# Kernel optimization log

Measured on AMD Instinct MI355X. Metric: run time of the kernel, lower is better.

## Reference

```python
import jax, jax.numpy as jnp
import numpy as np

EPS = 1e-5

def _ln(x, g=None, b=None):
    m = jnp.mean(x, axis=-1, keepdims=True)
    v = jnp.var(x, axis=-1, keepdims=True)
    y = (x - m) / jnp.sqrt(v + EPS)
    if g is not None:
        y = y * g + b
    return y

def setup_inputs() -> dict:
    key = jax.random.key(0)
    B, N, C = 2, 2048, 1024   # batch, tokens, query_dim
    H, D = 16, 64             # heads, dim_head -> inner = 1024
    inner = H * D
    ks = jax.random.split(key, 8)
    s = C ** -0.5
    inp = {
        'x':   jax.random.normal(ks[0], (B, N, C), jnp.float32),
        'w_q': jax.random.normal(ks[1], (C, inner), jnp.float32) * s,
        'b_q': jnp.zeros((inner,), jnp.float32),
        'w_k': jax.random.normal(ks[2], (C, inner), jnp.float32) * s,
        'b_k': jnp.zeros((inner,), jnp.float32),
        'w_v': jax.random.normal(ks[3], (C, inner), jnp.float32) * s,
        'b_v': jnp.zeros((inner,), jnp.float32),
        'g_q': jnp.ones((inner,), jnp.float32),
        'be_q': jnp.zeros((inner,), jnp.float32),
        'g_k': jnp.ones((inner,), jnp.float32),
        'be_k': jnp.zeros((inner,), jnp.float32),
        # to_out is zero-initialized in the torch code; use small random weights
        # so forward/backward are non-trivial for correctness testing.
        'w_o': jax.random.normal(ks[4], (inner, C), jnp.float32) * s,
        'b_o': jnp.zeros((C,), jnp.float32),
    }
    return inp

def reference(x, w_q, b_q, w_k, b_k, w_v, b_v, g_q, be_q, g_k, be_k, w_o, b_o):
    B, N, C = x.shape
    inner = w_q.shape[1]
    H = 16
    D = inner // H
    xn = _ln(x)                                  # pre-norm, no affine
    ctx = xn                                     # self-attention (context=None)
    silu = jax.nn.silu
    q = silu(xn) @ w_q + b_q                     # [B,N,inner]
    k = silu(ctx) @ w_k + b_k
    v = silu(ctx) @ w_v + b_v
    q = _ln(q, g_q, be_q)
    k = _ln(k, g_k, be_k)
    q = q * (inner ** -0.5)                      # NB: scale by inner_dim, pre-split
    q = q.reshape(B, N, H, D)
    k = k.reshape(B, N, H, D)
    v = v.reshape(B, N, H, D)
    w = jnp.einsum('bihd,bjhd->bhij', q, k)      # [B,H,N,N]
    w = jax.nn.softmax(w, axis=-1)
    o = jnp.einsum('bhij,bjhd->bihd', w, v).reshape(B, N, inner)
    return silu(o) @ w_o + b_o
```

## Files before the change

kernel.cpp:

```cpp
#include <hip/hip_runtime.h>
#include <hip/hip_bf16.h>
#include <math.h>

#define LN_EPS 1e-5f

typedef __attribute__((ext_vector_type(8))) short bf16x8;
typedef __attribute__((ext_vector_type(8))) short short8;
typedef __attribute__((ext_vector_type(4))) float f32x4;
typedef unsigned short ushort_t;

__device__ __forceinline__ float silu_f(float x) {
    return x / (1.0f + __expf(-x));
}

__device__ __forceinline__ ushort_t f2bf(float f) {
    __hip_bfloat16 h = __float2bfloat16(f);
    return *reinterpret_cast<ushort_t*>(&h);
}

__device__ __forceinline__ float bf2f(ushort_t u) {
    __hip_bfloat16 h = *reinterpret_cast<__hip_bfloat16*>(&u);
    return __bfloat162float(h);
}

__device__ __forceinline__ unsigned pk2(float a, float b) {
    unsigned r;
    asm("v_cvt_pk_bf16_f32 %0, %1, %2" : "=v"(r) : "v"(a), "v"(b));
    return r;
}

__device__ __forceinline__ float fast_exp2(float x) {
#if defined(__has_builtin)
#if __has_builtin(__builtin_amdgcn_exp2f)
    return __builtin_amdgcn_exp2f(x);
#else
    return exp2f(x);
#endif
#else
    return exp2f(x);
#endif
}

__device__ __forceinline__ void gld16(const void* g, void* lds) {
    __builtin_amdgcn_global_load_lds(
        (const __attribute__((address_space(1))) unsigned int*)g,
        (__attribute__((address_space(3))) unsigned int*)lds, 16, 0, 0);
}

__device__ __forceinline__ float2 block_reduce2(float2 p, float2* sbuf) {
    #pragma unroll
    for (int off = 32; off > 0; off >>= 1) {
        p.x += __shfl_down(p.x, off, 64);
        p.y += __shfl_down(p.y, off, 64);
    }
    int lane = threadIdx.x & 63;
    int wid  = threadIdx.x >> 6;
    if (lane == 0) sbuf[wid] = p;
    __syncthreads();
    if (threadIdx.x == 0) {
        float2 r = sbuf[0];
        for (int i = 1; i < 4; ++i) { r.x += sbuf[i].x; r.y += sbuf[i].y; }
        sbuf[0] = r;
    }
    __syncthreads();
    return sbuf[0];
}

__global__ __launch_bounds__(256) void ln_silu_kernel(
    const float* __restrict__ x, ushort_t* __restrict__ out)
{
    __shared__ float2 sbuf[4];
    const int C = 1024;
    int row = blockIdx.x;
    const float4* xr = (const float4*)(x + (size_t)row * C);
    float4 v = xr[threadIdx.x];
    float2 p;
    p.x = v.x + v.y + v.z + v.w;
    p.y = v.x*v.x + v.y*v.y + v.z*v.z + v.w*v.w;
    float2 s = block_reduce2(p, sbuf);
    float mean = s.x / (float)C;
    float var  = s.y / (float)C - mean * mean;
    float rstd = rsqrtf(var + LN_EPS);
    ushort4 y;
    y.x = f2bf(silu_f((v.x - mean) * rstd));
    y.y = f2bf(silu_f((v.y - mean) * rstd));
    y.z = f2bf(silu_f((v.z - mean) * rstd));
    y.w = f2bf(silu_f((v.w - mean) * rstd));
    ((ushort4*)(out + (size_t)row * C))[threadIdx.x] = y;
}

__global__ __launch_bounds__(256) void ln_affine_bf16(
    ushort_t* __restrict__ qk0, ushort_t* __restrict__ qk1,
    const float* __restrict__ g0, const float* __restrict__ be0,
    const float* __restrict__ g1, const float* __restrict__ be1,
    float scale0, float scale1)
{
    __shared__ float2 sbuf[4];
    const int C = 1024;
    int which = blockIdx.y;
    ushort_t* q = which ? qk1 : qk0;
    const float* g  = which ? g1  : g0;
    const float* be = which ? be1 : be0;
    float scale = which ? scale1 : scale0;
    int row = blockIdx.x;
    ushort4 u = ((ushort4*)(q + (size_t)row * C))[threadIdx.x];
    float v0 = bf2f(u.x), v1 = bf2f(u.y), v2 = bf2f(u.z), v3 = bf2f(u.w);
    float2 p;
    p.x = v0 + v1 + v2 + v3;
    p.y = v0*v0 + v1*v1 + v2*v2 + v3*v3;
    float2 s = block_reduce2(p, sbuf);
    float mean = s.x / (float)C;
    float var  = s.y / (float)C - mean * mean;
    float rstd = rsqrtf(var + LN_EPS);
    float4 gv = ((const float4*)g)[threadIdx.x];
    float4 bv = ((const float4*)be)[threadIdx.x];
    ushort4 y;
    y.x = f2bf(((v0 - mean) * rstd * gv.x + bv.x) * scale);
    y.y = f2bf(((v1 - mean) * rstd * gv.y + bv.y) * scale);
    y.z = f2bf(((v2 - mean) * rstd * gv.z + bv.z) * scale);
    y.w = f2bf(((v3 - mean) * rstd * gv.w + bv.w) * scale);
    ((ushort4*)(q + (size_t)row * C))[threadIdx.x] = y;
}

struct W4 { const float* p[4]; };

__global__ __launch_bounds__(256) void transpose_w(W4 w, ushort_t* __restrict__ outbase)
{
    __shared__ float Ls[64][65];
    int z = blockIdx.z;
    const float* in = w.p[z];
    ushort_t* out = outbase + (size_t)z * 1024 * 1024;
    int r0 = blockIdx.y * 64, c0 = blockIdx.x * 64;
    int t = threadIdx.x, r = t >> 2, j = (t & 3) * 16;
    #pragma unroll
    for (int i = 0; i < 4; ++i) {
        float4 v = *(const float4*)(in + (size_t)(r0 + r) * 1024 + c0 + j + i * 4);
        Ls[r][j + i*4 + 0] = v.x;
        Ls[r][j + i*4 + 1] = v.y;
        Ls[r][j + i*4 + 2] = v.z;
        Ls[r][j + i*4 + 3] = v.w;
    }
    __syncthreads();
    __align__(16) ushort_t tmp[16];
    #pragma unroll
    for (int i = 0; i < 16; ++i) tmp[i] = f2bf(Ls[j + i][r]);
    ushort_t* op = out + (size_t)(c0 + r) * 1024 + r0 + j;
    *(short8*)(op)     = *(short8*)(tmp);
    *(short8*)(op + 8) = *(short8*)(tmp + 8);
}

template<int BM, bool OUT_BF16>
__global__ __launch_bounds__(256) void gemm_mfma(
    const ushort_t* __restrict__ A, const ushort_t* __restrict__ Bt0,
    const float* __restrict__ b0, const float* __restrict__ b1,
    const float* __restrict__ b2, void* __restrict__ out0,
    ushort_t* __restrict__ vt_out,
    int M, int N, int K)
{
    constexpr int BK = 64;
    constexpr int MI = BM / 32;
    __shared__ ushort_t Smem[(BM + 128) * BK];
    ushort_t* As = Smem;
    ushort_t* Bs = Smem + BM * BK;

    int z = blockIdx.z;
    const ushort_t* Bt = Bt0 + (size_t)z * N * K;
    const float* bias = (z == 0) ? b0 : (z == 1) ? b1 : b2;

    int t = threadIdx.x;
    int lane = t & 63, wv = t >> 6;
    int wr = wv >> 1, wc = wv & 1;
    int quad = lane >> 4, ln16 = lane & 15;

    int row0 = blockIdx.y * BM;
    int col0 = blockIdx.x * 128;

    const f32x4 zero4 = {0.f, 0.f, 0.f, 0.f};
    f32x4 acc[MI][4];
    #pragma unroll
    for (int i = 0; i < MI; ++i)
        #pragma unroll
        for (int j = 0; j < 4; ++j) acc[i][j] = zero4;

    for (int kt = 0; kt < K; kt += BK) {
        #pragma unroll
        for (int c = 0; c < BM / 32; ++c) {
            int idx = c * 256 + t;
            int r = idx >> 3, ch = idx & 7;
            int g = ch ^ (r & 7);
            gld16(A + (size_t)(row0 + r) * K + kt + g * 8,
                  As + (size_t)(c * 256 + wv * 64) * 8);
        }
        #pragma unroll
        for (int c = 0; c < 4; ++c) {
            int idx = c * 256 + t;
            int r = idx >> 3, ch = idx & 7;
            int g = ch ^ (r & 7);
            gld16(Bt + (size_t)(col0 + r) * K + kt + g * 8,
                  Bs + (size_t)(c * 256 + wv * 64) * 8);
        }
        __syncthreads();
        #pragma unroll
        for (int s = 0; s < 2; ++s) {
            bf16x8 af[MI], bf[4];
            int g = s * 4 + quad;
            #pragma unroll
            for (int i = 0; i < MI; ++i) {
                int m = wr * (BM / 2) + i * 16 + ln16;
                af[i] = *(const bf16x8*)(As + (size_t)(m * 8 + (g ^ (m & 7))) * 8);
            }
            #pragma unroll
            for (int j = 0; j < 4; ++j) {
                int n = wc * 64 + j * 16 + ln16;
                bf[j] = *(const bf16x8*)(Bs + (size_t)(n * 8 + (g ^ (n & 7))) * 8);
            }
            #pragma unroll
            for (int i = 0; i < MI; ++i)
                #pragma unroll
                for (int j = 0; j < 4; ++j)
                    acc[i][j] = __builtin_amdgcn_mfma_f32_16x16x32_bf16(
                        af[i], bf[j], acc[i][j], 0, 0, 0);
        }
        __syncthreads();
    }

    if (OUT_BF16 && z == 2 && BM == 128) {
        ushort_t* tb = Smem + wv * 4096;
        int tok0 = row0 + wr * 64;
        int chn0 = col0 + wc * 64;
        #pragma unroll
        for (int j = 0; j < 4; ++j) {
            int chl = j * 16 + ln16;
            float bv = bias[chn0 + chl];
            #pragma unroll
            for (int i = 0; i < MI; ++i) {
                uint2 uu;
                uu.x = pk2(acc[i][j][0] + bv, acc[i][j][1] + bv);
                uu.y = pk2(acc[i][j][2] + bv, acc[i][j][3] + bv);
                int hc = i * 4 + quad;
                int phys = hc ^ ((chl & 7) << 1);
                *(uint2*)(tb + chl * 64 + phys * 4) = uu;
            }
        }
        int bb2 = tok0 >> 11;
        int tokb = tok0 & 2047;
        #pragma unroll
        for (int p = 0; p < 8; ++p) {
            int chl = p * 8 + (lane >> 3);
            int tc  = lane & 7;
            int ptc = tc ^ (chl & 7);
            uint4 vvv = *(const uint4*)(tb + chl * 64 + ptc * 8);
            *(uint4*)(vt_out + ((size_t)bb2 * 1024 + chn0 + chl) * 2048 + tokb + tc * 8) = vvv;
        }
    } else {
        #pragma unroll
        for (int j = 0; j < 4; ++j) {
            int col = col0 + wc * 64 + j * 16 + ln16;
            float bv = bias[col];
            #pragma unroll
            for (int i = 0; i < MI; ++i) {
                int rowb = row0 + wr * (BM / 2) + i * 16 + quad * 4;
                #pragma unroll
                for (int r = 0; r < 4; ++r) {
                    float val = acc[i][j][r] + bv;
                    if (OUT_BF16) {
                        ushort_t* out = (ushort_t*)out0 + (size_t)z * M * N;
                        out[(size_t)(rowb + r) * N + col] = f2bf(val);
                    } else {
                        float* out = (float*)out0;
                        out[(size_t)(rowb + r) * N + col] = val;
                    }
                }
            }
        }
    }
}

__global__ __launch_bounds__(256, 4) void flash_mfma(
    const ushort_t* __restrict__ qb, const ushort_t* __restrict__ kb,
    const ushort_t* __restrict__ vT, ushort_t* __restrict__ ob)
{
    const int N = 2048, HD = 1024, D = 64, H = 16;
    const int KT = 64;
    const int NT = N / KT;
    __shared__ ushort_t Ks[2][64 * 64];
    __shared__ ushort_t Vs[2][64 * 64];

    int t = threadIdx.x, lane = t & 63, wv = t >> 6;
    int quad = lane >> 4, ln16 = lane & 15;
    int qt = blockIdx.x, h = blockIdx.y, b = blockIdx.z;

    size_t qk_base = (size_t)b * N * HD + (size_t)h * D;
    size_t vt_base = (size_t)(b * H + h) * D * N;

    bf16x8 qf[2];
    {
        const ushort_t* qp = qb + qk_base + (size_t)(qt * 64 + wv * 16 + ln16) * HD;
        qf[0] = *(const bf16x8*)(qp + quad * 8);
        qf[1] = *(const bf16x8*)(qp + 32 + quad * 8);
    }

    bf16x8 ones;
    #pragma unroll
    for (int i = 0; i < 8; ++i) ones[i] = (short)0x3F80;

    const f32x4 zero4 = {0.f, 0.f, 0.f, 0.f};
    f32x4 oacc[4];
    f32x4 lacc = zero4;
    #pragma unroll
    for (int j = 0; j < 4; ++j) oacc[j] = zero4;

    auto stage_K = [&](ushort_t* KsB, int kt) {
        #pragma unroll
        for (int c = 0; c < 2; ++c) {
            int idx = c * 256 + t;
            int r = idx >> 3, ch = idx & 7, g = ch ^ (r & 7);
            int pr = (r & ~31) | (((r >> 2) & 3) << 3) | (((r >> 4) & 1) << 2) | (r & 3);
            gld16(kb + qk_base + (size_t)(kt + pr) * HD + g * 8,
                  KsB + (size_t)(c * 256 + wv * 64) * 8);
        }
    };
    auto stage_V = [&](ushort_t* VsB, int kt) {
        #pragma unroll
        for (int c = 0; c < 2; ++c) {
            int idx = c * 256 + t;
            int r = idx >> 3, ch = idx & 7, g = ch ^ (r & 7);
            gld16(vT + vt_base + (size_t)r * N + kt + g * 8,
                  VsB + (size_t)(c * 256 + wv * 64) * 8);
        }
    };

    auto qk_tile = [&](const ushort_t* KsB, f32x4 (&st)[4]) {
        #pragma unroll
        for (int j = 0; j < 4; ++j) st[j] = zero4;
        __builtin_amdgcn_s_setprio(1);
        #pragma unroll
        for (int s = 0; s < 2; ++s) {
            int g = s * 4 + quad;
            #pragma unroll
            for (int j = 0; j < 4; ++j) {
                int n = j * 16 + ln16;
                bf16x8 kf = *(const bf16x8*)(KsB + ((size_t)n * 8 + (g ^ (n & 7))) * 8);
                st[j] = __builtin_amdgcn_mfma_f32_16x16x32_bf16(kf, qf[s], st[j], 0, 0, 0);
            }
        }
        __builtin_amdgcn_s_setprio(0);
    };

    auto sm_pv = [&](f32x4 (&st)[4], const ushort_t* VsB) {
        bf16x8 vf[2][4];
        #pragma unroll
        for (int w = 0; w < 2; ++w) {
            int phys = (w * 4 + quad) ^ (ln16 & 7);
            #pragma unroll
            for (int mt = 0; mt < 4; ++mt)
                vf[w][mt] = *(const bf16x8*)(VsB + (size_t)(mt * 16 + ln16) * 64 + phys * 8);
        }
        #pragma unroll
        for (int j = 0; j < 4; ++j) {
            st[j][0] = fast_exp2(st[j][0]);
            st[j][1] = fast_exp2(st[j][1]);
            st[j][2] = fast_exp2(st[j][2]);
            st[j][3] = fast_exp2(st[j][3]);
        }
        #pragma unroll
        for (int w = 0; w < 2; ++w) {
            uint4 up;
            up.x = pk2(st[2*w][0],   st[2*w][1]);
            up.y = pk2(st[2*w][2],   st[2*w][3]);
            up.z = pk2(st[2*w+1][0], st[2*w+1][1]);
            up.w = pk2(st[2*w+1][2], st[2*w+1][3]);
            bf16x8 pf = __builtin_bit_cast(bf16x8, up);
            __builtin_amdgcn_s_setprio(1);
            lacc = __builtin_amdgcn_mfma_f32_16x16x32_bf16(ones, pf, lacc, 0, 0, 0);
            #pragma unroll
            for (int mt = 0; mt < 4; ++mt)
                oacc[mt] = __builtin_amdgcn_mfma_f32_16x16x32_bf16(vf[w][mt], pf, oacc[mt], 0, 0, 0);
            __builtin_amdgcn_s_setprio(0);
        }
    };

    f32x4 stA[4], stB[4];

    stage_K(Ks[0], 0);       stage_V(Vs[0], 0);
    stage_K(Ks[1], KT);      stage_V(Vs[1], KT);
    asm volatile("s_waitcnt vmcnt(4)" ::: "memory");
    __builtin_amdgcn_s_barrier();
    __builtin_amdgcn_sched_barrier(0);
    qk_tile(Ks[0], stA);
    __builtin_amdgcn_sched_barrier(0);
    __builtin_amdgcn_s_barrier();

    #pragma unroll 1
    for (int it = 0; it < NT - 2; it += 2) {
        stage_K(Ks[0], (it + 2) * KT);
        asm volatile("s_waitcnt vmcnt(4)" ::: "memory");
        __builtin_amdgcn_s_barrier();
        __builtin_amdgcn_sched_barrier(0);
        qk_tile(Ks[1], stB);
        sm_pv(stA, Vs[0]);
        __builtin_amdgcn_sched_barrier(0);
        __builtin_amdgcn_s_barrier();
        stage_V(Vs[0], (it + 2) * KT);

        stage_K(Ks[1], (it + 3) * KT);
        asm volatile("s_waitcnt vmcnt(4)" ::: "memory");
        __builtin_amdgcn_s_barrier();
        __builtin_amdgcn_sched_barrier(0);
        qk_tile(Ks[0], stA);
        sm_pv(stB, Vs[1]);
        __builtin_amdgcn_sched_barrier(0);
        __builtin_amdgcn_s_barrier();
        stage_V(Vs[1], (it + 3) * KT);
    }

    asm volatile("s_waitcnt vmcnt(2)" ::: "memory");
    __builtin_amdgcn_s_barrier();
    __builtin_amdgcn_sched_barrier(0);
    qk_tile(Ks[1], stB);
    sm_pv(stA, Vs[0]);
    asm volatile("s_waitcnt vmcnt(0)" ::: "memory");
    __builtin_amdgcn_s_barrier();
    __builtin_amdgcn_sched_barrier(0);
    sm_pv(stB, Vs[1]);

    float inv = 1.0f / lacc[0];
    size_t rowoff = qk_base + (size_t)(qt * 64 + wv * 16 + ln16) * HD;
    #pragma unroll
    for (int mt = 0; mt < 4; ++mt) {
        float o0 = silu_f(oacc[mt][0] * inv);
        float o1 = silu_f(oacc[mt][1] * inv);
        float o2 = silu_f(oacc[mt][2] * inv);
        float o3 = silu_f(oacc[mt][3] * inv);
        uint2 uu;
        uu.x = pk2(o0, o1);
        uu.y = pk2(o2, o3);
        *(uint2*)(ob + rowoff + mt * 16 + quad * 4) = uu;
    }
}

extern "C" void kernel_launch(void* const* d_in, const int* in_sizes, int n_in,
                              void* d_out, int out_size, void* d_ws, size_t ws_size,
                              hipStream_t stream) {
    const float* x    = (const float*)d_in[0];
    const float* w_q  = (const float*)d_in[1];
    const float* b_q  = (const float*)d_in[2];
    const float* w_k  = (const float*)d_in[3];
    const float* b_k  = (const float*)d_in[4];
    const float* w_v  = (const float*)d_in[5];
    const float* b_v  = (const float*)d_in[6];
    const float* g_q  = (const float*)d_in[7];
    const float* be_q = (const float*)d_in[8];
    const float* g_k  = (const float*)d_in[9];
    const float* be_k = (const float*)d_in[10];
    const float* w_o  = (const float*)d_in[11];
    const float* b_o  = (const float*)d_in[12];
    float* out = (float*)d_out;

    const int B = 2, N = 2048, C = 1024, H = 16, INNER = 1024;
    const int M = B * N;
    const size_t MC = (size_t)M * C;

    ushort_t* ws  = (ushort_t*)d_ws;
    ushort_t* sx  = ws;
    ushort_t* qkv = ws + MC;
    ushort_t* vTp = ws + 4 * MC;
    ushort_t* wT  = ws + 5 * MC;

    ushort_t* qbuf = qkv;
    ushort_t* kbuf = qkv + MC;
    ushort_t* obuf = sx;

    W4 w4; w4.p[0] = w_q; w4.p[1] = w_k; w4.p[2] = w_v; w4.p[3] = w_o;
    transpose_w<<<dim3(16, 16, 4), 256, 0, stream>>>(w4, wT);

    ln_silu_kernel<<<M, 256, 0, stream>>>(x, sx);

    gemm_mfma<128, true><<<dim3(INNER / 128, M / 128, 3), 256, 0, stream>>>(
        sx, wT, b_q, b_k, b_v, qkv, vTp, M, INNER, C);

    ln_affine_bf16<<<dim3(M, 2), 256, 0, stream>>>(
        qbuf, kbuf, g_q, be_q, g_k, be_k, 0.03125f * 1.44269504f, 1.0f);

    flash_mfma<<<dim3(N / 64, H, B), 256, 0, stream>>>(qbuf, kbuf, vTp, obuf);

    gemm_mfma<64, false><<<dim3(C / 128, M / 64, 1), 256, 0, stream>>>(
        obuf, wT + (size_t)3 * 1024 * 1024, b_o, b_o, b_o, out, nullptr, M, C, INNER);
}
```

Measured before the change: 227.7 us.

## Double-buffer LDS tiles in MFMA GEMM to overlap global loads with compute

The GEMM main loop now uses two LDS buffers. The next K-tile's direct-to-LDS global loads are issued before computing the current tile, and explicit vmcnt waits plus barriers replace the full __syncthreads pair. MFMA blocks are wrapped in s_setprio to favour the compute waves. This is meant to hide global memory latency, at the cost of doubling LDS use, which may lower occupancy; it also assumes K/BK is even.

New measurement: 203.2 us. 10.7% less time.

```diff
diff --git a/kernel.cpp b/kernel.cpp
--- a/kernel.cpp
+++ b/kernel.cpp
@@ -159,9 +159,12 @@
 {
     constexpr int BK = 64;
     constexpr int MI = BM / 32;
-    __shared__ ushort_t Smem[(BM + 128) * BK];
-    ushort_t* As = Smem;
-    ushort_t* Bs = Smem + BM * BK;
+    constexpr int LOADS = BM / 32 + 4;
+    __shared__ ushort_t Smem[2 * (BM + 128) * BK];
+    ushort_t* As0 = Smem;
+    ushort_t* Bs0 = Smem + BM * BK;
+    ushort_t* As1 = Smem + (BM + 128) * BK;
+    ushort_t* Bs1 = As1 + BM * BK;
 
     int z = blockIdx.z;
     const ushort_t* Bt = Bt0 + (size_t)z * N * K;
@@ -182,14 +185,14 @@
         #pragma unroll
         for (int j = 0; j < 4; ++j) acc[i][j] = zero4;
 
-    for (int kt = 0; kt < K; kt += BK) {
+    auto stage = [&](ushort_t* AsB, ushort_t* BsB, int kt) {
         #pragma unroll
         for (int c = 0; c < BM / 32; ++c) {
             int idx = c * 256 + t;
             int r = idx >> 3, ch = idx & 7;
             int g = ch ^ (r & 7);
             gld16(A + (size_t)(row0 + r) * K + kt + g * 8,
-                  As + (size_t)(c * 256 + wv * 64) * 8);
+                  AsB + (size_t)(c * 256 + wv * 64) * 8);
         }
         #pragma unroll
         for (int c = 0; c < 4; ++c) {
@@ -197,9 +200,11 @@
             int r = idx >> 3, ch = idx & 7;
             int g = ch ^ (r & 7);
             gld16(Bt + (size_t)(col0 + r) * K + kt + g * 8,
-                  Bs + (size_t)(c * 256 + wv * 64) * 8);
-        }
-        __syncthreads();
+                  BsB + (size_t)(c * 256 + wv * 64) * 8);
+        }
+    };
+
+    auto compute = [&](const ushort_t* AsB, const ushort_t* BsB) {
         #pragma unroll
         for (int s = 0; s < 2; ++s) {
             bf16x8 af[MI], bf[4];
@@ -207,21 +212,52 @@
             #pragma unroll
             for (int i = 0; i < MI; ++i) {
                 int m = wr * (BM / 2) + i * 16 + ln16;
-                af[i] = *(const bf16x8*)(As + (size_t)(m * 8 + (g ^ (m & 7))) * 8);
+                af[i] = *(const bf16x8*)(AsB + (size_t)(m * 8 + (g ^ (m & 7))) * 8);
             }
             #pragma unroll
             for (int j = 0; j < 4; ++j) {
                 int n = wc * 64 + j * 16 + ln16;
-                bf[j] = *(const bf16x8*)(Bs + (size_t)(n * 8 + (g ^ (n & 7))) * 8);
+                bf[j] = *(const bf16x8*)(BsB + (size_t)(n * 8 + (g ^ (n & 7))) * 8);
             }
+            __builtin_amdgcn_s_setprio(1);
             #pragma unroll
             for (int i = 0; i < MI; ++i)
                 #pragma unroll
                 for (int j = 0; j < 4; ++j)
                     acc[i][j] = __builtin_amdgcn_mfma_f32_16x16x32_bf16(
                         af[i], bf[j], acc[i][j], 0, 0, 0);
-        }
-        __syncthreads();
+            __builtin_amdgcn_s_setprio(0);
+        }
+    };
+
+    auto wait_prev = [&]() {
+        if constexpr (BM == 128) asm volatile("s_waitcnt vmcnt(8)" ::: "memory");
+        else                     asm volatile("s_waitcnt vmcnt(6)" ::: "memory");
+    };
+
+    const int NTk = K / BK;
+    stage(As0, Bs0, 0);
+    #pragma unroll 1
+    for (int it = 0; it < NTk; it += 2) {
+        stage(As1, Bs1, (it + 1) * BK);
+        wait_prev();
+        __builtin_amdgcn_s_barrier();
+        __builtin_amdgcn_sched_barrier(0);
+        compute(As0, Bs0);
+        __builtin_amdgcn_sched_barrier(0);
+        __builtin_amdgcn_s_barrier();
+
+        if (it + 2 < NTk) {
+            stage(As0, Bs0, (it + 2) * BK);
+            wait_prev();
+        } else {
+            asm volatile("s_waitcnt vmcnt(0)" ::: "memory");
+        }
+        __builtin_amdgcn_s_barrier();
+        __builtin_amdgcn_sched_barrier(0);
+        compute(As1, Bs1);
+        __builtin_amdgcn_sched_barrier(0);
+        __builtin_amdgcn_s_barrier();
     }
 
     if (OUT_BF16 && z == 2 && BM == 128) {
```
